# Performance work log

Hardware: AMD Instinct MI355X
Metric: run time of the kernel (lower is better)

Reference implementation:

```python
import jax, jax.numpy as jnp
import numpy as np

B, N, D, H, T, NHOP = 128, 256, 512, 512, 8, 1
NEG = -1e18


def _attn_score(feat, query, v, w):
    # feat: [B, Ns, H], query: [B, Nq, H] -> score [B, Nq, Ns]
    s = jnp.tanh(feat[:, None, :, :] + jnp.matmul(query, w)[:, :, None, :])
    return jnp.einsum('bqnh,h->bqn', s, v)


def _lstm(x, h0, c0, w_ih, w_hh, b_ih, b_hh):
    # x: [B, L, D]; torch nn.LSTM gate order i, f, g, o
    def step(carry, xt):
        h, c = carry
        g = xt @ w_ih.T + h @ w_hh.T + b_ih + b_hh
        i, f, gg, o = jnp.split(g, 4, axis=-1)
        c = jax.nn.sigmoid(f) * c + jax.nn.sigmoid(i) * jnp.tanh(gg)
        h = jax.nn.sigmoid(o) * jnp.tanh(c)
        return (h, c), h
    _, hs = jax.lax.scan(step, (h0, c0), jnp.swapaxes(x, 0, 1))
    return jnp.swapaxes(hs, 0, 1)  # [B, L, H]


def setup_inputs():
    key = jax.random.key(0)
    ks = jax.random.split(key, 17)
    INI = 0.01
    return {
        'attn_mem': jax.random.normal(ks[0], (B, N, D), jnp.float32),
        'lstm_in': jax.random.normal(ks[1], (B, T, D), jnp.float32),
        'mem_sizes': jax.random.randint(ks[2], (B,), 1, N + 1).astype(jnp.int32),
        'init_h': jax.random.uniform(ks[3], (H,), jnp.float32, -INI, INI),
        'init_c': jax.random.uniform(ks[4], (H,), jnp.float32, -INI, INI),
        'init_i': jax.random.uniform(ks[5], (D,), jnp.float32, -0.1, 0.1),
        'stop': jax.random.uniform(ks[6], (D,), jnp.float32, -INI, INI),
        'w_ih': jax.random.normal(ks[7], (4 * H, D), jnp.float32) * 0.02,
        'w_hh': jax.random.normal(ks[8], (4 * H, H), jnp.float32) * 0.02,
        'b_ih': jnp.zeros((4 * H,), jnp.float32),
        'b_hh': jnp.zeros((4 * H,), jnp.float32),
        'attn_wm': jax.random.normal(ks[9], (D, H), jnp.float32) * 0.02,
        'attn_wq': jax.random.normal(ks[10], (H, H), jnp.float32) * 0.02,
        'attn_v': jax.random.uniform(ks[11], (H,), jnp.float32, -INI, INI),
        'hop_wm': jax.random.normal(ks[12], (D, H), jnp.float32) * 0.02,
        'hop_wq': jax.random.normal(ks[13], (H, H), jnp.float32) * 0.02,
        'hop_v': jax.random.uniform(ks[14], (H,), jnp.float32, -INI, INI),
    }


def reference(attn_mem, lstm_in, mem_sizes, init_h, init_c, init_i, stop,
              w_ih, w_hh, b_ih, b_hh, attn_wm, attn_wq, attn_v,
              hop_wm, hop_wq, hop_v):
    b = attn_mem.shape[0]
    # append stop slot: zeros row, scatter-add stop vector at index mem_sizes[i]
    mem = jnp.concatenate([attn_mem, jnp.zeros((b, 1, D), attn_mem.dtype)], axis=1)
    mem = mem.at[jnp.arange(b), mem_sizes].add(stop)
    sizes = mem_sizes + 1
    # _prepare
    attn_feat = mem @ attn_wm   # [B, N+1, H]
    hop_feat = mem @ hop_wm     # [B, N+1, H]
    x = jnp.concatenate([jnp.broadcast_to(init_i, (b, 1, D)), lstm_in], axis=1)
    h0 = jnp.broadcast_to(init_h, (b, H))
    c0 = jnp.broadcast_to(init_c, (b, H))
    query = _lstm(x, h0, c0, w_ih, w_hh, b_ih, b_hh)  # [B, T+1, H]
    # n_hop masked glimpse attention
    mask = jnp.arange(N + 1)[None, :] < sizes[:, None]  # [B, N+1]
    for _ in range(NHOP):
        score = _attn_score(hop_feat, query, hop_v, hop_wq)
        score = jnp.where(mask[:, None, :], score, NEG)
        query = jnp.einsum('bqn,bnh->bqh', jax.nn.softmax(score, axis=-1), hop_feat)
    # final unmasked pointer scores [B, T+1, N+1]
    return _attn_score(attn_feat, query, attn_v, attn_wq)
```

## Files before the change

kernel.cpp:

```cpp
#include <hip/hip_runtime.h>
#include <hip/hip_bf16.h>
#include <math.h>

#define BB   128
#define NPTS 256
#define NP1  257
#define DD   512
#define HH   512
#define G4   2048
#define TP1  9
#define NEGF -1e18f
#define MTOT (BB * NP1)
#define CSC  2.8853900817779268f
#define L2E  1.4426950408889634f

typedef __attribute__((ext_vector_type(8))) short bf16x8;
typedef __attribute__((ext_vector_type(8))) unsigned short u16x8;
typedef __attribute__((ext_vector_type(4))) float f32x4;

__device__ __forceinline__ float bf2f(unsigned short u)
{
    union { unsigned int i; float f; } x;
    x.i = (unsigned int)u << 16;
    return x.f;
}

__device__ __forceinline__ float sigm(float x)
{
    return __builtin_amdgcn_rcpf(1.0f + __builtin_amdgcn_exp2f(-x * L2E));
}

__device__ __forceinline__ float fast_tanh(float x)
{
    float e = __builtin_amdgcn_exp2f(x * CSC);
    return 1.0f - 2.0f * __builtin_amdgcn_rcpf(e + 1.0f);
}

__device__ __forceinline__ void gl_lds16(const __hip_bfloat16* g, __hip_bfloat16* l)
{
    __builtin_amdgcn_global_load_lds(
        (const __attribute__((address_space(1))) void*)g,
        (__attribute__((address_space(3))) void*)l, 16, 0, 0);
}

__device__ __forceinline__ void stage8(const __hip_bfloat16* const* aptr,
                                       const __hip_bfloat16* const* bptr,
                                       const int* ldsoff,
                                       __hip_bfloat16* A_, __hip_bfloat16* B_, int kt)
{
#pragma unroll
    for (int s = 0; s < 4; ++s) gl_lds16(aptr[s] + kt, A_ + ldsoff[s]);
#pragma unroll
    for (int s = 0; s < 4; ++s) gl_lds16(bptr[s] + kt, B_ + ldsoff[s]);
}

__device__ __forceinline__ void gemm_step(const __hip_bfloat16* A_,
                                          const __hip_bfloat16* B_,
                                          f32x4 (&acc)[4][4],
                                          int wr, int wc, int rA, int kgrp)
{
#pragma unroll
    for (int ks = 0; ks < 2; ++ks) {
        bf16x8 af[4], bfr[4];
#pragma unroll
        for (int fi = 0; fi < 4; ++fi) {
            const int r = wr + fi * 16 + rA;
            const int ch = (ks * 4 + kgrp) ^ (r & 7);
            af[fi] = *(const bf16x8*)(A_ + r * 64 + ch * 8);
        }
#pragma unroll
        for (int fj = 0; fj < 4; ++fj) {
            const int r = wc + fj * 16 + rA;
            const int ch = (ks * 4 + kgrp) ^ (r & 7);
            bfr[fj] = *(const bf16x8*)(B_ + r * 64 + ch * 8);
        }
#pragma unroll
        for (int fi = 0; fi < 4; ++fi)
#pragma unroll
            for (int fj = 0; fj < 4; ++fj)
                acc[fi][fj] = __builtin_amdgcn_mfma_f32_16x16x32_bf16(
                    af[fi], bfr[fj], acc[fi][fj], 0, 0, 0);
    }
}

__global__ __launch_bounds__(256)
void k_prep(const float* __restrict__ hop_wm, const float* __restrict__ attn_wm,
            const float* __restrict__ hop_wq, const float* __restrict__ attn_wq,
            const float* __restrict__ w_ih, const float* __restrict__ w_hh,
            const float* __restrict__ b_ih, const float* __restrict__ b_hh,
            const float* __restrict__ stop, const float* __restrict__ lstm_in,
            const float* __restrict__ init_i, const float* __restrict__ init_h,
            const float* __restrict__ init_c, const float* __restrict__ Amem,
            __hip_bfloat16* __restrict__ Wt2, __hip_bfloat16* __restrict__ WqtH,
            __hip_bfloat16* __restrict__ WqtA, __hip_bfloat16* __restrict__ wih_bf,
            __hip_bfloat16* __restrict__ whh_bf, float* __restrict__ bsum,
            float* __restrict__ stopm2, __hip_bfloat16* __restrict__ Xbf,
            __hip_bfloat16* __restrict__ h_a, float* __restrict__ cbuf,
            __hip_bfloat16* __restrict__ Abf)
{
    const int x = blockIdx.x, t = threadIdx.x;
    if (x < 1024) {
        const float* W = (x < 512) ? hop_wm : attn_wm;
        const int col = x & 511;
        Wt2[(size_t)x * DD + t]       = __float2bfloat16(CSC * W[(size_t)t * HH + col]);
        Wt2[(size_t)x * DD + t + 256] = __float2bfloat16(CSC * W[(size_t)(t + 256) * HH + col]);
    } else if (x < 2048) {
        const int j = x - 1024;
        if (j < 512) {
            WqtH[(size_t)j * DD + t]       = __float2bfloat16(CSC * hop_wq[(size_t)t * HH + j]);
            WqtH[(size_t)j * DD + t + 256] = __float2bfloat16(CSC * hop_wq[(size_t)(t + 256) * HH + j]);
        } else {
            const int jj = j - 512;
            WqtA[(size_t)jj * DD + t]       = __float2bfloat16(attn_wq[(size_t)t * HH + jj]);
            WqtA[(size_t)jj * DD + t + 256] = __float2bfloat16(attn_wq[(size_t)(t + 256) * HH + jj]);
        }
    } else if (x < 4096) {
        const size_t r = (size_t)(x - 2048) * DD;
        wih_bf[r + t]       = __float2bfloat16(w_ih[r + t]);
        wih_bf[r + t + 256] = __float2bfloat16(w_ih[r + t + 256]);
    } else if (x < 6144) {
        const size_t r = (size_t)(x - 4096) * DD;
        whh_bf[r + t]       = __float2bfloat16(w_hh[r + t]);
        whh_bf[r + t + 256] = __float2bfloat16(w_hh[r + t + 256]);
    } else if (x == 6144) {
#pragma unroll
        for (int i = 0; i < 8; ++i) {
            const int idx = t + 256 * i;
            bsum[idx] = b_ih[idx] + b_hh[idx];
        }
    } else if (x < 6149) {
        const int h = (x - 6145) * 256 + t;
        const float* W = (h < 512) ? hop_wm : attn_wm;
        const int col = h & 511;
        float a = 0.f;
        for (int k = 0; k < DD; ++k) a += stop[k] * W[(size_t)k * HH + col];
        stopm2[h] = CSC * a;
    } else if (x < 7301) {
        const int m = x - 6149;
        const int bb = m / TP1, tt = m - bb * TP1;
        const float* src = (tt == 0) ? init_i : (lstm_in + (size_t)(bb * 8 + tt - 1) * DD);
        float2 vv = *(const float2*)(src + 2 * t);
        __hip_bfloat16* o = Xbf + (size_t)m * DD + 2 * t;
        o[0] = __float2bfloat16(vv.x);
        o[1] = __float2bfloat16(vv.y);
    } else if (x < 7557) {
        const int idx = (x - 7301) * 256 + t;
        h_a[idx]  = __float2bfloat16(init_h[idx & (HH - 1)]);
        cbuf[idx] = init_c[idx & (HH - 1)];
    } else {
        const int m = (x - 7557) * 2 + (t >> 7);
        const int b = m / NP1;
        const int n = m - b * NP1;
        const int c4 = (t & 127) * 4;
        float4 v = make_float4(0.f, 0.f, 0.f, 0.f);
        if (n < NPTS)
            v = *(const float4*)(Amem + ((size_t)(b * NPTS + n)) * DD + c4);
        __hip_bfloat16* o = Abf + (size_t)m * DD + c4;
        o[0] = __float2bfloat16(v.x);
        o[1] = __float2bfloat16(v.y);
        o[2] = __float2bfloat16(v.z);
        o[3] = __float2bfloat16(v.w);
    }
}

__global__ __launch_bounds__(256)
void k_feat2(const __hip_bfloat16* __restrict__ A,
             const __hip_bfloat16* __restrict__ Bt,
             const float* __restrict__ stopm2,
             const int* __restrict__ msz,
             __hip_bfloat16* __restrict__ E2)
{
    const int orig = blockIdx.x;
    const int wgid = (orig & 7) * 257 + (orig >> 3);
    const int m0 = (wgid >> 3) * 128;
    const int n0 = (wgid & 7) * 128;

    __shared__ __align__(16) __hip_bfloat16 SM[4][128 * 64];
    __hip_bfloat16* As0 = SM[0];
    __hip_bfloat16* Bs0 = SM[1];
    __hip_bfloat16* As1 = SM[2];
    __hip_bfloat16* Bs1 = SM[3];
    const int tid  = threadIdx.x;
    const int lane = tid & 63;
    const int wid  = tid >> 6;
    const int wr = (wid >> 1) * 64;
    const int wc = (wid & 1) * 64;

    const __hip_bfloat16* aptr[4];
    const __hip_bfloat16* bptr[4];
    int ldsoff[4];
#pragma unroll
    for (int s = 0; s < 4; ++s) {
        const int si = wid * 4 + s;
        const int o = si * 1024 + lane * 16;
        const int row = o >> 7;
        const int chunk = (o >> 4) & 7;
        const int sch = chunk ^ (row & 7);
        aptr[s] = A + (size_t)(m0 + row) * DD + sch * 8;
        bptr[s] = Bt + (size_t)(n0 + row) * DD + sch * 8;
        ldsoff[s] = si * 512;
    }

    f32x4 acc[4][4];
#pragma unroll
    for (int i = 0; i < 4; ++i)
#pragma unroll
        for (int j = 0; j < 4; ++j) acc[i][j] = (f32x4){0.f, 0.f, 0.f, 0.f};

    const int rA = lane & 15;
    const int kgrp = lane >> 4;

    stage8(aptr, bptr, ldsoff, As0, Bs0, 0);
    __syncthreads();
    for (int kt = 0; kt < DD; kt += 128) {
        stage8(aptr, bptr, ldsoff, As1, Bs1, kt + 64);
        gemm_step(As0, Bs0, acc, wr, wc, rA, kgrp);
        __syncthreads();
        if (kt + 128 < DD) stage8(aptr, bptr, ldsoff, As0, Bs0, kt + 128);
        gemm_step(As1, Bs1, acc, wr, wc, rA, kgrp);
        __syncthreads();
    }

#pragma unroll
    for (int fi = 0; fi < 4; ++fi) {
#pragma unroll
        for (int r = 0; r < 4; ++r) {
            const int m = m0 + wr + fi * 16 + (lane >> 4) * 4 + r;
            const int b = m / NP1;
            const int n = m - b * NP1;
            const bool addstop = (n == msz[b]);
#pragma unroll
            for (int fj = 0; fj < 4; ++fj) {
                const int h = n0 + wc + fj * 16 + (lane & 15);
                float v = acc[fi][fj][r];
                if (addstop) v += stopm2[h];
                E2[(size_t)m * 1024 + h] = __float2bfloat16(__builtin_amdgcn_exp2f(v));
            }
        }
    }
}

__global__ __launch_bounds__(256)
void k_gemm_bt(const __hip_bfloat16* __restrict__ A,
               const __hip_bfloat16* __restrict__ Bt,
               const float* __restrict__ bias,
               float* __restrict__ C, int ldc, int expout)
{
    __shared__ __align__(16) __hip_bfloat16 SM[4][128 * 64];
    __hip_bfloat16* As0 = SM[0];
    __hip_bfloat16* Bs0 = SM[1];
    __hip_bfloat16* As1 = SM[2];
    __hip_bfloat16* Bs1 = SM[3];
    const int tid  = threadIdx.x;
    const int lane = tid & 63;
    const int wid  = tid >> 6;
    const int m0 = blockIdx.x * 128;
    const int n0 = blockIdx.y * 128;
    const int wr = (wid >> 1) * 64;
    const int wc = (wid & 1) * 64;

    const __hip_bfloat16* aptr[4];
    const __hip_bfloat16* bptr[4];
    int ldsoff[4];
#pragma unroll
    for (int s = 0; s < 4; ++s) {
        const int si = wid * 4 + s;
        const int o = si * 1024 + lane * 16;
        const int row = o >> 7;
        const int chunk = (o >> 4) & 7;
        const int sch = chunk ^ (row & 7);
        aptr[s] = A + (size_t)(m0 + row) * DD + sch * 8;
        bptr[s] = Bt + (size_t)(n0 + row) * DD + sch * 8;
        ldsoff[s] = si * 512;
    }

    f32x4 acc[4][4];
#pragma unroll
    for (int i = 0; i < 4; ++i)
#pragma unroll
        for (int j = 0; j < 4; ++j) acc[i][j] = (f32x4){0.f, 0.f, 0.f, 0.f};

    const int rA = lane & 15;
    const int kgrp = lane >> 4;

    stage8(aptr, bptr, ldsoff, As0, Bs0, 0);
    __syncthreads();
    for (int kt = 0; kt < DD; kt += 128) {
        stage8(aptr, bptr, ldsoff, As1, Bs1, kt + 64);
        gemm_step(As0, Bs0, acc, wr, wc, rA, kgrp);
        __syncthreads();
        if (kt + 128 < DD) stage8(aptr, bptr, ldsoff, As0, Bs0, kt + 128);
        gemm_step(As1, Bs1, acc, wr, wc, rA, kgrp);
        __syncthreads();
    }

#pragma unroll
    for (int fi = 0; fi < 4; ++fi) {
#pragma unroll
        for (int r = 0; r < 4; ++r) {
            const int m = m0 + wr + fi * 16 + (lane >> 4) * 4 + r;
#pragma unroll
            for (int fj = 0; fj < 4; ++fj) {
                const int h = n0 + wc + fj * 16 + (lane & 15);
                float v = acc[fi][fj][r];
                if (bias) v += bias[h];
                if (expout) v = __builtin_amdgcn_exp2f(v);
                C[(size_t)m * ldc + h] = v;
            }
        }
    }
}

__global__ __launch_bounds__(256)
void k_lstm2(const __hip_bfloat16* __restrict__ hin,
             const __hip_bfloat16* __restrict__ whh,
             const float* __restrict__ gx,
             float* __restrict__ cbuf,
             __hip_bfloat16* __restrict__ hout,
             __hip_bfloat16* __restrict__ query,
             int t)
{
    __shared__ __align__(16) __hip_bfloat16 As[64 * 512];
    __shared__ __align__(16) __hip_bfloat16 Bs[32 * 512];
    __shared__ float Gs[64][36];
    const int tid  = threadIdx.x;
    const int lane = tid & 63;
    const int wid  = tid >> 6;
    const int m0  = blockIdx.x * 64;
    const int hc0 = blockIdx.y * 8;
    const int wy = wid >> 1, wx = wid & 1;

#pragma unroll
    for (int i = 0; i < 16; ++i) {
        const int o = (i * 256 + tid) * 16;
        const int c = o >> 13;
        const int oc = o & 8191;
        const int row = oc >> 7;
        const int ch = (oc >> 4) & 7;
        const int sch = ch ^ (row & 7);
        gl_lds16(hin + (size_t)(m0 + row) * HH + c * 64 + sch * 8, As + (o >> 1));
    }
#pragma unroll
    for (int i = 0; i < 8; ++i) {
        const int o = (i * 256 + tid) * 16;
        const int c = o >> 12;
        const int oc = o & 4095;
        const int row = oc >> 7;
        const int ch = (oc >> 4) & 7;
        const int sch = ch ^ (row & 7);
        const int brow = (row >> 3) * 512 + hc0 + (row & 7);
        gl_lds16(whh + (size_t)brow * HH + c * 64 + sch * 8, Bs + (o >> 1));
    }
    __syncthreads();

    f32x4 acc[2];
    acc[0] = (f32x4){0.f, 0.f, 0.f, 0.f};
    acc[1] = (f32x4){0.f, 0.f, 0.f, 0.f};
    const int rr = lane & 15;
    const int kg = lane >> 4;

#pragma unroll
    for (int ks = 0; ks < 16; ++ks) {
        const int c = ks >> 1, sub = ks & 1;
        const __hip_bfloat16* Ab = As + c * 4096;
        const __hip_bfloat16* Bb = Bs + c * 2048;
        const int rb = wx * 16 + rr;
        const bf16x8 bfr = *(const bf16x8*)(Bb + rb * 64 + (((sub * 4 + kg) ^ (rb & 7)) * 8));
#pragma unroll
        for (int fi = 0; fi < 2; ++fi) {
            const int ra = wy * 32 + fi * 16 + rr;
            const bf16x8 af = *(const bf16x8*)(Ab + ra * 64 + (((sub * 4 + kg) ^ (ra & 7)) * 8));
            acc[fi] = __builtin_amdgcn_mfma_f32_16x16x32_bf16(af, bfr, acc[fi], 0, 0, 0);
        }
    }

#pragma unroll
    for (int fi = 0; fi < 2; ++fi)
#pragma unroll
        for (int r = 0; r < 4; ++r)
            Gs[wy * 32 + fi * 16 + (lane >> 4) * 4 + r][wx * 16 + (lane & 15)] = acc[fi][r];
    __syncthreads();

    const int j  = tid & 7;
    const int mg = tid >> 3;
#pragma unroll
    for (int mi = 0; mi < 2; ++mi) {
        const int m = mg * 2 + mi;
        const float* gxr = gx + ((size_t)(m0 + m) * TP1 + t) * G4 + hc0 + j;
        float iv = sigm(Gs[m][j]      + gxr[0]);
        float fv = sigm(Gs[m][8 + j]  + gxr[512]);
        float gv = fast_tanh(Gs[m][16 + j] + gxr[1024]);
        float ov = sigm(Gs[m][24 + j] + gxr[1536]);
        const int ci = (m0 + m) * HH + hc0 + j;
        float cv = fv * cbuf[ci] + iv * gv;
        float hv = ov * fast_tanh(cv);
        cbuf[ci] = cv;
        hout[ci] = __float2bfloat16(hv);
        query[((size_t)(m0 + m) * TP1 + t) * HH + hc0 + j] = __float2bfloat16(hv);
    }
}

__global__ __launch_bounds__(256)
void k_score(const __hip_bfloat16* __restrict__ E2, int efoff,
             const float* __restrict__ Eq,
             const float* __restrict__ v, const int* __restrict__ msz,
             float* __restrict__ score, int masked)
{
    const int wid  = threadIdx.x >> 6;
    const int lane = threadIdx.x & 63;
    const int n = blockIdx.x * 4 + wid;
    const int b = blockIdx.y;
    if (n >= NP1) return;
    float* sp = score + (size_t)b * TP1 * NP1 + n;
    if (masked && n > msz[b]) {
        if (lane == 0)
#pragma unroll
            for (int q = 0; q < TP1; ++q) sp[q * NP1] = NEGF;
        return;
    }
    const u16x8 fu = *(const u16x8*)((const unsigned short*)E2
                                     + ((size_t)b * NP1 + n) * 1024 + efoff + lane * 8);
    float ef[8];
#pragma unroll
    for (int i = 0; i < 8; ++i) ef[i] = bf2f(fu[i]);
    const float4* v4 = (const float4*)v;
    const float4 va = v4[lane * 2], vb = v4[lane * 2 + 1];
    const float vs8 = va.x + va.y + va.z + va.w + vb.x + vb.y + vb.z + vb.w;
    float v2[8] = {2.f*va.x, 2.f*va.y, 2.f*va.z, 2.f*va.w,
                   2.f*vb.x, 2.f*vb.y, 2.f*vb.z, 2.f*vb.w};
    for (int q = 0; q < TP1; ++q) {
        const float4* q4 = (const float4*)(Eq + ((size_t)b * TP1 + q) * HH);
        const float4 qa = q4[lane * 2], qb = q4[lane * 2 + 1];
        float eq[8] = {qa.x, qa.y, qa.z, qa.w, qb.x, qb.y, qb.z, qb.w};
        float acc = 0.f;
#pragma unroll
        for (int i = 0; i < 8; ++i)
            acc = fmaf(v2[i], __builtin_amdgcn_rcpf(fmaf(ef[i], eq[i], 1.0f)), acc);
        float s = vs8 - acc;
#pragma unroll
        for (int off = 32; off; off >>= 1) s += __shfl_down(s, off);
        if (lane == 0) sp[q * NP1] = s;
    }
}

__global__ __launch_bounds__(256)
void k_softpv(const float* __restrict__ score, const __hip_bfloat16* __restrict__ E2,
              const int* __restrict__ msz, __hip_bfloat16* __restrict__ outq)
{
    const int b   = blockIdx.x;
    const int ch  = blockIdx.y;
    const int tid = threadIdx.x;
    const int lane = tid & 63, wid = tid >> 6;
    __shared__ float p[TP1][NP1 + 3];
    __shared__ float comb[TP1][256];
    const int nlim = msz[b] + 1;

    const float* sb = score + (size_t)b * TP1 * NP1;
    for (int q = wid; q < TP1; q += 4) {
        const float* srow = sb + q * NP1;
        float mx = NEGF;
        for (int n = lane; n < nlim; n += 64) mx = fmaxf(mx, srow[n]);
#pragma unroll
        for (int off = 32; off; off >>= 1) mx = fmaxf(mx, __shfl_xor(mx, off));
        float sum = 0.f;
        for (int n = lane; n < nlim; n += 64) {
            float e = __builtin_amdgcn_exp2f((srow[n] - mx) * L2E);
            p[q][n] = e;
            sum += e;
        }
#pragma unroll
        for (int off = 32; off; off >>= 1) sum += __shfl_xor(sum, off);
        float inv = 1.f / sum;
        for (int n = lane; n < nlim; n += 64) p[q][n] *= inv;
    }
    __syncthreads();

    const int ng = tid >> 7;
    const int tc = tid & 127;
    const int col = ch * 256 + tc * 2;
    const unsigned short* fb = (const unsigned short*)E2 + (size_t)b * NP1 * 1024 + col;
    float a0[TP1] = {}, a1[TP1] = {};
    for (int n = ng; n < nlim; n += 2) {
        const unsigned int u = *(const unsigned int*)(fb + (size_t)n * 1024);
        const float f0 = __builtin_amdgcn_logf(bf2f((unsigned short)(u & 0xffffu)));
        const float f1 = __builtin_amdgcn_logf(bf2f((unsigned short)(u >> 16)));
#pragma unroll
        for (int q = 0; q < TP1; ++q) {
            const float pq = p[q][n];
            a0[q] += pq * f0;
            a1[q] += pq * f1;
        }
    }
    if (ng == 1) {
#pragma unroll
        for (int q = 0; q < TP1; ++q) {
            comb[q][tc * 2]     = a0[q];
            comb[q][tc * 2 + 1] = a1[q];
        }
    }
    __syncthreads();
    if (ng == 0) {
        __hip_bfloat16* oq = outq + (size_t)(b * TP1) * HH + col;
#pragma unroll
        for (int q = 0; q < TP1; ++q) {
            oq[(size_t)q * HH]     = __float2bfloat16(a0[q] + comb[q][tc * 2]);
            oq[(size_t)q * HH + 1] = __float2bfloat16(a1[q] + comb[q][tc * 2 + 1]);
        }
    }
}

extern "C" void kernel_launch(void* const* d_in, const int* in_sizes, int n_in,
                              void* d_out, int out_size, void* d_ws, size_t ws_size,
                              hipStream_t stream)
{
    const float* attn_mem  = (const float*)d_in[0];
    const float* lstm_in   = (const float*)d_in[1];
    const int*   mem_sizes = (const int*)d_in[2];
    const float* init_h    = (const float*)d_in[3];
    const float* init_c    = (const float*)d_in[4];
    const float* init_i    = (const float*)d_in[5];
    const float* stop      = (const float*)d_in[6];
    const float* w_ih      = (const float*)d_in[7];
    const float* w_hh      = (const float*)d_in[8];
    const float* b_ih      = (const float*)d_in[9];
    const float* b_hh      = (const float*)d_in[10];
    const float* attn_wm   = (const float*)d_in[11];
    const float* attn_wq   = (const float*)d_in[12];
    const float* attn_v    = (const float*)d_in[13];
    const float* hop_wm    = (const float*)d_in[14];
    const float* hop_wq    = (const float*)d_in[15];
    const float* hop_v     = (const float*)d_in[16];
    float* out = (float*)d_out;

    char* w = (char*)d_ws;
    __hip_bfloat16* Abf    = (__hip_bfloat16*)w;  w += (size_t)MTOT * DD * 2;
    __hip_bfloat16* E2     = (__hip_bfloat16*)w;  w += (size_t)MTOT * 1024 * 2;
    __hip_bfloat16* Xbf    = (__hip_bfloat16*)w;  w += (size_t)BB * TP1 * DD * 2;
    __hip_bfloat16* Wt2    = (__hip_bfloat16*)w;  w += (size_t)1024 * DD * 2;
    __hip_bfloat16* WqtH   = (__hip_bfloat16*)w;  w += (size_t)HH * HH * 2;
    __hip_bfloat16* WqtA   = (__hip_bfloat16*)w;  w += (size_t)HH * HH * 2;
    __hip_bfloat16* wih_bf = (__hip_bfloat16*)w;  w += (size_t)G4 * DD * 2;
    __hip_bfloat16* whh_bf = (__hip_bfloat16*)w;  w += (size_t)G4 * HH * 2;
    __hip_bfloat16* h_a    = (__hip_bfloat16*)w;  w += (size_t)BB * HH * 2;
    __hip_bfloat16* h_b    = (__hip_bfloat16*)w;  w += (size_t)BB * HH * 2;
    __hip_bfloat16* query  = (__hip_bfloat16*)w;  w += (size_t)BB * TP1 * HH * 2;
    __hip_bfloat16* query2 = (__hip_bfloat16*)w;  w += (size_t)BB * TP1 * HH * 2;
    float* gatesx  = (float*)w;  w += (size_t)BB * TP1 * G4 * 4;
    float* eq      = (float*)w;  w += (size_t)BB * TP1 * HH * 4;
    float* score   = (float*)w;  w += (size_t)BB * TP1 * NP1 * 4;
    float* cbuf    = (float*)w;  w += (size_t)BB * HH * 4;
    float* stopm2  = (float*)w;  w += 1024 * 4;
    float* bsum    = (float*)w;  w += G4 * 4;

    k_prep<<<dim3(24005), dim3(256), 0, stream>>>(
        hop_wm, attn_wm, hop_wq, attn_wq, w_ih, w_hh, b_ih, b_hh,
        stop, lstm_in, init_i, init_h, init_c, attn_mem,
        Wt2, WqtH, WqtA, wih_bf, whh_bf, bsum, stopm2, Xbf, h_a, cbuf, Abf);

    k_feat2<<<dim3(2056), dim3(256), 0, stream>>>(Abf, Wt2, stopm2, mem_sizes, E2);

    k_gemm_bt<<<dim3(9, 16), dim3(256), 0, stream>>>(Xbf, wih_bf, bsum, gatesx, G4, 0);
    for (int t = 0; t < TP1; ++t) {
        const __hip_bfloat16* hin = (t & 1) ? h_b : h_a;
        __hip_bfloat16*      hout = (t & 1) ? h_a : h_b;
        k_lstm2<<<dim3(2, 64), dim3(256), 0, stream>>>(hin, whh_bf, gatesx, cbuf, hout, query, t);
    }

    k_gemm_bt<<<dim3(9, 4), dim3(256), 0, stream>>>(query, WqtH, nullptr, eq, HH, 1);
    k_score<<<dim3(65, 128), dim3(256), 0, stream>>>(E2, 0, eq, hop_v, mem_sizes, score, 1);
    k_softpv<<<dim3(128, 2), dim3(256), 0, stream>>>(score, E2, mem_sizes, query2);

    k_gemm_bt<<<dim3(9, 4), dim3(256), 0, stream>>>(query2, WqtA, nullptr, eq, HH, 1);
    k_score<<<dim3(65, 128), dim3(256), 0, stream>>>(E2, 512, eq, attn_v, mem_sizes, out, 0);
}
```

Before: 274.6 us.

## Transpose weights via LDS tiles and fully unroll GEMM load pipeline with vmcnt waits

```diff
diff --git a/kernel.cpp b/kernel.cpp
--- a/kernel.cpp
+++ b/kernel.cpp
@@ -82,6 +82,26 @@
                     af[fi], bfr[fj], acc[fi][fj], 0, 0, 0);
     }
 }
+
+#define PIPE_ITER(I, NW, Acur, Bcur, Anxt, Bnxt)                              \
+    if ((I) < 7) stage8(aptr, bptr, ldsoff, Anxt, Bnxt, ((I) + 1) * 64);      \
+    asm volatile("s_waitcnt vmcnt(" NW ")" ::: "memory");                     \
+    __builtin_amdgcn_s_barrier();                                             \
+    asm volatile("" ::: "memory");                                            \
+    gemm_step(Acur, Bcur, acc, wr, wc, rA, kgrp);                             \
+    __builtin_amdgcn_s_barrier();                                             \
+    asm volatile("" ::: "memory");
+
+#define PIPE_RUN()                                                            \
+    stage8(aptr, bptr, ldsoff, As0, Bs0, 0);                                  \
+    PIPE_ITER(0, "8", As0, Bs0, As1, Bs1)                                     \
+    PIPE_ITER(1, "8", As1, Bs1, As0, Bs0)                                     \
+    PIPE_ITER(2, "8", As0, Bs0, As1, Bs1)                                     \
+    PIPE_ITER(3, "8", As1, Bs1, As0, Bs0)                                     \
+    PIPE_ITER(4, "8", As0, Bs0, As1, Bs1)                                     \
+    PIPE_ITER(5, "8", As1, Bs1, As0, Bs0)                                     \
+    PIPE_ITER(6, "8", As0, Bs0, As1, Bs1)                                     \
+    PIPE_ITER(7, "0", As1, Bs1, As0, Bs0)
 
 __global__ __launch_bounds__(256)
 void k_prep(const float* __restrict__ hop_wm, const float* __restrict__ attn_wm,
@@ -99,56 +119,67 @@
             __hip_bfloat16* __restrict__ Abf)
 {
     const int x = blockIdx.x, t = threadIdx.x;
-    if (x < 1024) {
-        const float* W = (x < 512) ? hop_wm : attn_wm;
-        const int col = x & 511;
-        Wt2[(size_t)x * DD + t]       = __float2bfloat16(CSC * W[(size_t)t * HH + col]);
-        Wt2[(size_t)x * DD + t + 256] = __float2bfloat16(CSC * W[(size_t)(t + 256) * HH + col]);
-    } else if (x < 2048) {
-        const int j = x - 1024;
-        if (j < 512) {
-            WqtH[(size_t)j * DD + t]       = __float2bfloat16(CSC * hop_wq[(size_t)t * HH + j]);
-            WqtH[(size_t)j * DD + t + 256] = __float2bfloat16(CSC * hop_wq[(size_t)(t + 256) * HH + j]);
-        } else {
-            const int jj = j - 512;
-            WqtA[(size_t)jj * DD + t]       = __float2bfloat16(attn_wq[(size_t)t * HH + jj]);
-            WqtA[(size_t)jj * DD + t + 256] = __float2bfloat16(attn_wq[(size_t)(t + 256) * HH + jj]);
-        }
-    } else if (x < 4096) {
-        const size_t r = (size_t)(x - 2048) * DD;
-        wih_bf[r + t]       = __float2bfloat16(w_ih[r + t]);
-        wih_bf[r + t + 256] = __float2bfloat16(w_ih[r + t + 256]);
-    } else if (x < 6144) {
-        const size_t r = (size_t)(x - 4096) * DD;
-        whh_bf[r + t]       = __float2bfloat16(w_hh[r + t]);
-        whh_bf[r + t + 256] = __float2bfloat16(w_hh[r + t + 256]);
-    } else if (x == 6144) {
+    if (x < 256) {
+        __shared__ float S[64][69];
+        const int mat  = x >> 6;
+        const int tile = x & 63;
+        const int tr = tile >> 3, tc = tile & 7;
+        const float* W = (mat == 0) ? hop_wm : (mat == 1) ? attn_wm
+                       : (mat == 2) ? hop_wq : attn_wq;
+        __hip_bfloat16* O = (mat == 0) ? Wt2 : (mat == 1) ? (Wt2 + (size_t)512 * DD)
+                          : (mat == 2) ? WqtH : WqtA;
+        const float scale = (mat == 3) ? 1.0f : CSC;
+#pragma unroll
+        for (int k = 0; k < 4; ++k) {
+            const int r = (t >> 4) + k * 16;
+            const int c4 = (t & 15) * 4;
+            const float4 v = *(const float4*)(W + (size_t)(tr * 64 + r) * 512 + tc * 64 + c4);
+            S[r][c4] = v.x; S[r][c4 + 1] = v.y; S[r][c4 + 2] = v.z; S[r][c4 + 3] = v.w;
+        }
+        __syncthreads();
+        const int oc = tc * 64 + (t >> 2);
+        const int j0 = (t & 3) * 16;
+        __hip_bfloat16 tmp[16];
+#pragma unroll
+        for (int j = 0; j < 16; ++j)
+            tmp[j] = __float2bfloat16(scale * S[j0 + j][t >> 2]);
+        *(bf16x8*)(O + (size_t)oc * 512 + tr * 64 + j0)     = *(bf16x8*)&tmp[0];
+        *(bf16x8*)(O + (size_t)oc * 512 + tr * 64 + j0 + 8) = *(bf16x8*)&tmp[8];
+    } else if (x == 256) {
 #pragma unroll
         for (int i = 0; i < 8; ++i) {
             const int idx = t + 256 * i;
             bsum[idx] = b_ih[idx] + b_hh[idx];
         }
-    } else if (x < 6149) {
-        const int h = (x - 6145) * 256 + t;
+    } else if (x < 261) {
+        const int h = (x - 257) * 256 + t;
         const float* W = (h < 512) ? hop_wm : attn_wm;
         const int col = h & 511;
         float a = 0.f;
         for (int k = 0; k < DD; ++k) a += stop[k] * W[(size_t)k * HH + col];
         stopm2[h] = CSC * a;
-    } else if (x < 7301) {
-        const int m = x - 6149;
+    } else if (x < 1413) {
+        const int m = x - 261;
         const int bb = m / TP1, tt = m - bb * TP1;
         const float* src = (tt == 0) ? init_i : (lstm_in + (size_t)(bb * 8 + tt - 1) * DD);
         float2 vv = *(const float2*)(src + 2 * t);
         __hip_bfloat16* o = Xbf + (size_t)m * DD + 2 * t;
         o[0] = __float2bfloat16(vv.x);
         o[1] = __float2bfloat16(vv.y);
-    } else if (x < 7557) {
-        const int idx = (x - 7301) * 256 + t;
+    } else if (x < 1669) {
+        const int idx = (x - 1413) * 256 + t;
         h_a[idx]  = __float2bfloat16(init_h[idx & (HH - 1)]);
         cbuf[idx] = init_c[idx & (HH - 1)];
+    } else if (x < 3717) {
+        const size_t r = (size_t)(x - 1669) * DD;
+        wih_bf[r + t]       = __float2bfloat16(w_ih[r + t]);
+        wih_bf[r + t + 256] = __float2bfloat16(w_ih[r + t + 256]);
+    } else if (x < 5765) {
+        const size_t r = (size_t)(x - 3717) * DD;
+        whh_bf[r + t]       = __float2bfloat16(w_hh[r + t]);
+        whh_bf[r + t + 256] = __float2bfloat16(w_hh[r + t + 256]);
     } else {
-        const int m = (x - 7557) * 2 + (t >> 7);
+        const int m = (x - 5765) * 2 + (t >> 7);
         const int b = m / NP1;
         const int n = m - b * NP1;
         const int c4 = (t & 127) * 4;
@@ -210,16 +241,7 @@
     const int rA = lane & 15;
     const int kgrp = lane >> 4;
 
-    stage8(aptr, bptr, ldsoff, As0, Bs0, 0);
-    __syncthreads();
-    for (int kt = 0; kt < DD; kt += 128) {
-        stage8(aptr, bptr, ldsoff, As1, Bs1, kt + 64);
-        gemm_step(As0, Bs0, acc, wr, wc, rA, kgrp);
-        __syncthreads();
-        if (kt + 128 < DD) stage8(aptr, bptr, ldsoff, As0, Bs0, kt + 128);
-        gemm_step(As1, Bs1, acc, wr, wc, rA, kgrp);
-        __syncthreads();
-    }
+    PIPE_RUN()
 
 #pragma unroll
     for (int fi = 0; fi < 4; ++fi) {
@@ -283,16 +305,7 @@
     const int rA = lane & 15;
     const int kgrp = lane >> 4;
 
-    stage8(aptr, bptr, ldsoff, As0, Bs0, 0);
-    __syncthreads();
-    for (int kt = 0; kt < DD; kt += 128) {
-        stage8(aptr, bptr, ldsoff, As1, Bs1, kt + 64);
-        gemm_step(As0, Bs0, acc, wr, wc, rA, kgrp);
-        __syncthreads();
-        if (kt + 128 < DD) stage8(aptr, bptr, ldsoff, As0, Bs0, kt + 128);
-        gemm_step(As1, Bs1, acc, wr, wc, rA, kgrp);
-        __syncthreads();
-    }
+    PIPE_RUN()
 
 #pragma unroll
     for (int fi = 0; fi < 4; ++fi) {
@@ -552,7 +565,7 @@
     float* stopm2  = (float*)w;  w += 1024 * 4;
     float* bsum    = (float*)w;  w += G4 * 4;
 
-    k_prep<<<dim3(24005), dim3(256), 0, stream>>>(
+    k_prep<<<dim3(22213), dim3(256), 0, stream>>>(
         hop_wm, attn_wm, hop_wq, attn_wq, w_ih, w_hh, b_ih, b_hh,
         stop, lstm_in, init_i, init_h, init_c, attn_mem,
         Wt2, WqtH, WqtA, wih_bf, whh_bf, bsum, stopm2, Xbf, h_a, cbuf, Abf);
```

Result: faster. 264.6 us (-3.6%).
